# Performance work log

Measured on AMD Instinct MI355X. Metric: run time of the kernel, lower is better.

The kernel has to match this reference:

```python
import jax, jax.numpy as jnp
import numpy as np

N_FFT = 2048
HOP = 512
N_FREQ = N_FFT // 2 + 1  # 1025


def _dft_conv_weights():
    # periodic ('fftbins=True') Hann window, matching librosa get_window('hann', N, fftbins=True)
    n = np.arange(N_FFT)
    win = 0.5 - 0.5 * np.cos(2.0 * np.pi * n / N_FFT)
    k = np.arange(N_FREQ)
    ang = 2.0 * np.pi * np.outer(k, n) / N_FFT  # (F, n_fft)
    # W[n, k] = exp(-2*pi*i*n*k/N); real part = cos, imag part = -sin; windowed per-tap
    w_real = (np.cos(ang) * win[None, :]).astype(np.float32)
    w_imag = (-np.sin(ang) * win[None, :]).astype(np.float32)
    return w_real, w_imag


def setup_inputs() -> dict:
    key = jax.random.key(0)
    x = jax.random.normal(key, (16, 320000), dtype=jnp.float32)
    w_real, w_imag = _dft_conv_weights()
    return {
        "input": x,
        "conv_real_w": jnp.asarray(w_real),
        "conv_imag_w": jnp.asarray(w_imag),
    }


def reference(input, conv_real_w, conv_imag_w):
    # center=True: reflect-pad n_fft//2 on both sides
    pad = N_FFT // 2
    x = jnp.pad(input, ((0, 0), (pad, pad)), mode="reflect")  # (B, L + n_fft)
    L = x.shape[1]
    T = (L - N_FFT) // HOP + 1  # time_steps
    # frame extraction == Conv1d with kernel n_fft, stride hop
    idx = jnp.arange(T)[:, None] * HOP + jnp.arange(N_FFT)[None, :]  # (T, n_fft)
    frames = x[:, idx]  # (B, T, n_fft)
    real = jnp.einsum("btn,fn->bft", frames, conv_real_w)  # (B, F, T)
    imag = jnp.einsum("btn,fn->bft", frames, conv_imag_w)  # (B, F, T)
    return real, imag
```

## Files before the change

kernel.cpp:

```cpp
#include <hip/hip_runtime.h>

#define B_BATCH 16
#define XLEN    320000
#define NFFT    2048
#define HOP     512
#define PADW    1024
#define NFREQ   1025
#define T_OUT   626
#define M_ROWS  2050
#define NCOLS   (B_BATCH * T_OUT)
#define MT2     17
#define NT2     40
#define KT2     32

#define XPAD_LEN    322048
#define XPAD_STRIDE 330240
#define APACK_BYTES ((size_t)MT2 * KT2 * 2 * 8192)
#define XPAD_BYTES  ((size_t)(B_BATCH + 1) * XPAD_STRIDE * 2)
#define WS_NEEDED   (APACK_BYTES + XPAD_BYTES)

typedef __bf16 bf16x8 __attribute__((ext_vector_type(8)));
typedef __bf16 bf16x4 __attribute__((ext_vector_type(4)));
typedef float  f32x4  __attribute__((ext_vector_type(4)));

__device__ __forceinline__ void gload_lds16(const void* g, void* l) {
    __builtin_amdgcn_global_load_lds(
        (const __attribute__((address_space(1))) unsigned int*)g,
        (__attribute__((address_space(3))) unsigned int*)l,
        16, 0, 0);
}

__global__ __launch_bounds__(256) void prep_w(
    const float* __restrict__ wre, const float* __restrict__ wim,
    __bf16* __restrict__ apack)
{
    const int gid   = blockIdx.x * 256 + threadIdx.x;
    const int scell = gid & 3;
    const int row   = (gid >> 2) & 127;
    const int ks    = (gid >> 9) & 1;
    const int kt    = (gid >> 10) & 31;
    const int mt    = gid >> 15;

    const int grow = mt * 128 + row;
    const int k    = kt * 64 + ks * 32 + (((scell ^ (row >> 1)) & 3) << 3);

    bf16x8 v = bf16x8{};
    if (grow < M_ROWS) {
        const float* src = (grow < NFREQ)
            ? (wre + (size_t)grow * NFFT + k)
            : (wim + (size_t)(grow - NFREQ) * NFFT + k);
        const float4 a = *reinterpret_cast<const float4*>(src);
        const float4 b = *reinterpret_cast<const float4*>(src + 4);
        v[0] = (__bf16)a.x; v[1] = (__bf16)a.y; v[2] = (__bf16)a.z; v[3] = (__bf16)a.w;
        v[4] = (__bf16)b.x; v[5] = (__bf16)b.y; v[6] = (__bf16)b.z; v[7] = (__bf16)b.w;
    }
    *reinterpret_cast<bf16x8*>(apack + (size_t)gid * 8) = v;
}

__global__ __launch_bounds__(256) void prep_x(
    const float* __restrict__ x, __bf16* __restrict__ xpad)
{
    const int gid = blockIdx.x * 256 + threadIdx.x;
    if (gid >= (B_BATCH + 1) * (XPAD_STRIDE / 8)) return;
    const int b  = gid / (XPAD_STRIDE / 8);
    const int i0 = (gid - b * (XPAD_STRIDE / 8)) * 8;

    bf16x8 v = bf16x8{};
    if (b < B_BATCH) {
        const float* xb = x + (size_t)b * XLEN;
        const int pos0 = i0 - PADW;
        if (pos0 >= 0 && pos0 + 8 <= XLEN) {
            const float4 a = *reinterpret_cast<const float4*>(xb + pos0);
            const float4 c = *reinterpret_cast<const float4*>(xb + pos0 + 4);
            v[0] = (__bf16)a.x; v[1] = (__bf16)a.y; v[2] = (__bf16)a.z; v[3] = (__bf16)a.w;
            v[4] = (__bf16)c.x; v[5] = (__bf16)c.y; v[6] = (__bf16)c.z; v[7] = (__bf16)c.w;
        } else {
            #pragma unroll
            for (int e = 0; e < 8; ++e) {
                const int i = i0 + e;
                if (i >= XPAD_LEN) { v[e] = (__bf16)0.f; continue; }
                int p = i - PADW;
                p = (p < 0) ? -p : p;
                p = (p >= XLEN) ? (2 * XLEN - 2 - p) : p;
                v[e] = (__bf16)xb[p];
            }
        }
    }
    *reinterpret_cast<bf16x8*>(xpad + (size_t)b * XPAD_STRIDE + i0) = v;
}


#define MFMA16 __builtin_amdgcn_mfma_f32_16x16x32_bf16

#define VM3 asm volatile("s_waitcnt vmcnt(3)" ::: "memory");
#define VM0 asm volatile("s_waitcnt vmcnt(0)" ::: "memory");

#define STG(KT_, KS_, SLOT_) do {                                                  \
    gload_lds16(ablk + (((KT_) * 2 + (KS_)) << 13),                                \
                lds + ((SLOT_) << 13) + (wid << 10));                              \
    {                                                                              \
        const int koff = (KT_) * 128 + (KS_) * 64;                                 \
        unsigned char* d_ = lds + 24576 + ((SLOT_) << 14) + (wid << 10);           \
        gload_lds16(gb0 + koff, d_);                                               \
        gload_lds16(gb1 + koff, d_ + 8192);                                        \
    }                                                                              \
} while (0)

#define PH3(SLOT_, STAGE_, VMW_) do {                                              \
    VMW_                                                                           \
    __builtin_amdgcn_s_barrier();                                                  \
    __builtin_amdgcn_sched_barrier(0);                                             \
    const unsigned abase = ((SLOT_) << 13) + offA_base;                            \
    const unsigned bbase = 24576u + ((SLOT_) << 14) + offB_base;                   \
    bf16x8 a0 = *(const bf16x8*)(lds + abase);                                     \
    bf16x8 a1 = *(const bf16x8*)(lds + abase + 1024);                              \
    bf16x8 a2 = *(const bf16x8*)(lds + abase + 2048);                              \
    bf16x8 a3 = *(const bf16x8*)(lds + abase + 3072);                              \
    bf16x8 b0 = *(const bf16x8*)(lds + bbase);                                     \
    bf16x8 b1 = *(const bf16x8*)(lds + bbase + 1024);                              \
    bf16x8 b2 = *(const bf16x8*)(lds + bbase + 2048);                              \
    bf16x8 b3 = *(const bf16x8*)(lds + bbase + 3072);                              \
    STAGE_                                                                         \
    __builtin_amdgcn_s_setprio(1);                                                 \
    acc[0][0] = MFMA16(a0, b0, acc[0][0], 0, 0, 0);                                \
    acc[0][1] = MFMA16(a0, b1, acc[0][1], 0, 0, 0);                                \
    acc[0][2] = MFMA16(a0, b2, acc[0][2], 0, 0, 0);                                \
    acc[0][3] = MFMA16(a0, b3, acc[0][3], 0, 0, 0);                                \
    acc[1][0] = MFMA16(a1, b0, acc[1][0], 0, 0, 0);                                \
    acc[1][1] = MFMA16(a1, b1, acc[1][1], 0, 0, 0);                                \
    acc[1][2] = MFMA16(a1, b2, acc[1][2], 0, 0, 0);                                \
    acc[1][3] = MFMA16(a1, b3, acc[1][3], 0, 0, 0);                                \
    acc[2][0] = MFMA16(a2, b0, acc[2][0], 0, 0, 0);                                \
    acc[2][1] = MFMA16(a2, b1, acc[2][1], 0, 0, 0);                                \
    acc[2][2] = MFMA16(a2, b2, acc[2][2], 0, 0, 0);                                \
    acc[2][3] = MFMA16(a2, b3, acc[2][3], 0, 0, 0);                                \
    acc[3][0] = MFMA16(a3, b0, acc[3][0], 0, 0, 0);                                \
    acc[3][1] = MFMA16(a3, b1, acc[3][1], 0, 0, 0);                                \
    acc[3][2] = MFMA16(a3, b2, acc[3][2], 0, 0, 0);                                \
    acc[3][3] = MFMA16(a3, b3, acc[3][3], 0, 0, 0);                                \
    __builtin_amdgcn_s_setprio(0);                                                 \
} while (0)

__global__ __launch_bounds__(512, 4) void stft_gemm4(
    const __bf16* __restrict__ apack,
    const __bf16* __restrict__ xpad,
    float* __restrict__ out)
{
    __shared__ __align__(16) unsigned char lds[73728];

    const int tid  = threadIdx.x;
    const int lane = tid & 63;
    const int wid  = tid >> 6;
    const int wm   = wid >> 2;
    const int wn   = wid & 3;
    const int fr   = lane & 15;
    const int kq   = lane >> 4;

    const int orig = (blockIdx.x & 7) * 85 + (blockIdx.x >> 3);
    const int nt = orig / MT2;
    const int mt = orig % MT2;

    const char* ablk = (const char*)apack + (size_t)mt * (KT2 * 2 * 8192) + (size_t)tid * 16;

    const char* xpb = (const char*)xpad;
    const char* gb0;
    const char* gb1;
    {
        const int row0 = tid >> 2;
        const int sc   = ((tid & 3) ^ (row0 >> 1)) & 3;
        int col = nt * 256 + row0;
        unsigned b = (unsigned)col / 626u;
        int tc = col - (int)b * 626;
        gb0 = xpb + ((size_t)b * XPAD_STRIDE + (size_t)tc * 512) * 2 + sc * 16;
        col = nt * 256 + 128 + row0;
        b = (unsigned)col / 626u;
        tc = col - (int)b * 626;
        gb1 = xpb + ((size_t)b * XPAD_STRIDE + (size_t)tc * 512) * 2 + sc * 16;
    }

    const unsigned swz = (unsigned)(((kq ^ (fr >> 1)) & 3) << 4);
    const unsigned offA_base = (unsigned)((wm * 64 + fr) * 64) + swz;
    const unsigned offB_base = (unsigned)((wn * 64 + fr) * 64) + swz;

    f32x4 acc[4][4];
    #pragma unroll
    for (int m = 0; m < 4; ++m)
        #pragma unroll
        for (int n = 0; n < 4; ++n)
            acc[m][n] = f32x4{0.f, 0.f, 0.f, 0.f};

    STG(0, 0, 0);
    STG(0, 1, 1);

    #pragma unroll 1
    for (int i = 0; i < 10; ++i) {
        const int kb = 3 * i;
        PH3(0, STG(kb + 1, 0, 2);, VM3);
        PH3(1, STG(kb + 1, 1, 0);, VM3);
        PH3(2, STG(kb + 2, 0, 1);, VM3);
        PH3(0, STG(kb + 2, 1, 2);, VM3);
        PH3(1, STG(kb + 3, 0, 0);, VM3);
        PH3(2, STG(kb + 3, 1, 1);, VM3);
    }
    PH3(0, STG(31, 0, 2);, VM3);
    PH3(1, STG(31, 1, 0);, VM3);
    PH3(2, , VM3);
    PH3(0, , VM0);

    const size_t imag_base = (size_t)B_BATCH * NFREQ * T_OUT;
    #pragma unroll
    for (int n = 0; n < 4; ++n) {
        const int col = nt * 256 + wn * 64 + n * 16 + fr;
        if (col < NCOLS) {
            const unsigned b = (unsigned)col / 626u;
            const int tc = col - (int)b * 626;
            const size_t colbase = (size_t)b * NFREQ * T_OUT + (size_t)tc;
            #pragma unroll
            for (int m = 0; m < 4; ++m) {
                #pragma unroll
                for (int j = 0; j < 4; ++j) {
                    const int grow = mt * 128 + wm * 64 + m * 16 + kq * 4 + j;
                    if (grow < M_ROWS) {
                        const size_t off = (grow < NFREQ)
                            ? colbase + (size_t)grow * T_OUT
                            : imag_base + colbase + (size_t)(grow - NFREQ) * T_OUT;
                        out[off] = acc[m][n][j];
                    }
                }
            }
        }
    }
}

__device__ __forceinline__ unsigned lds_off_fb(int row, int kbyte) {
    return (unsigned)(row * 128 + (kbyte ^ ((row & 7) << 4)));
}

__global__ __launch_bounds__(256) void stft_gemm_fb(
    const float* __restrict__ x,
    const float* __restrict__ wre,
    const float* __restrict__ wim,
    float* __restrict__ out)
{
    __shared__ __align__(16) unsigned char ldsA[128 * 128];
    __shared__ __align__(16) unsigned char ldsB[128 * 128];

    const int tid  = threadIdx.x;
    const int lane = tid & 63;
    const int wid  = tid >> 6;
    const int wmf  = wid >> 1;
    const int wnf  = wid & 1;

    const int bid = blockIdx.x;
    const int b   = bid / (17 * 5);
    const int rem = bid % (17 * 5);
    const int mt  = rem / 5;
    const int nt  = rem % 5;

    const int row0 = mt * 128;
    const int col0 = nt * 128;
    const float* xb = x + (size_t)b * XLEN;

    const int c4 = (tid & 15) * 4;
    const int r0 = tid >> 4;

    f32x4 acc[4][4];
    #pragma unroll
    for (int m = 0; m < 4; ++m)
        #pragma unroll
        for (int n = 0; n < 4; ++n)
            acc[m][n] = f32x4{0.f, 0.f, 0.f, 0.f};

    const int fr = lane & 15;
    const int kq = lane >> 4;

    for (int k0 = 0; k0 < NFFT; k0 += 64) {
        bf16x4 sa[8], sb[8];
        #pragma unroll
        for (int rr = 0; rr < 8; ++rr) {
            const int row  = rr * 16 + r0;
            const int grow = row0 + row;
            float4 v = make_float4(0.f, 0.f, 0.f, 0.f);
            if (grow < M_ROWS) {
                const float* wsrc = (grow < NFREQ)
                    ? (wre + (size_t)grow * NFFT)
                    : (wim + (size_t)(grow - NFREQ) * NFFT);
                v = *reinterpret_cast<const float4*>(wsrc + k0 + c4);
            }
            sa[rr].x = (__bf16)v.x; sa[rr].y = (__bf16)v.y;
            sa[rr].z = (__bf16)v.z; sa[rr].w = (__bf16)v.w;
        }
        #pragma unroll
        for (int rr = 0; rr < 8; ++rr) {
            const int trow = rr * 16 + r0;
            const int t    = col0 + trow;
            float4 v = make_float4(0.f, 0.f, 0.f, 0.f);
            if (t < T_OUT) {
                const int pos = t * HOP + k0 + c4 - PADW;
                if (pos >= 0 && pos <= XLEN - 4) {
                    v = *reinterpret_cast<const float4*>(xb + pos);
                } else {
                    float tmp[4];
                    #pragma unroll
                    for (int e = 0; e < 4; ++e) {
                        int p = pos + e;
                        p = (p < 0) ? -p : p;
                        p = (p >= XLEN) ? (2 * XLEN - 2 - p) : p;
                        tmp[e] = xb[p];
                    }
                    v = make_float4(tmp[0], tmp[1], tmp[2], tmp[3]);
                }
            }
            sb[rr].x = (__bf16)v.x; sb[rr].y = (__bf16)v.y;
            sb[rr].z = (__bf16)v.z; sb[rr].w = (__bf16)v.w;
        }
        __syncthreads();
        #pragma unroll
        for (int rr = 0; rr < 8; ++rr) {
            const int row = rr * 16 + r0;
            *reinterpret_cast<bf16x4*>(ldsA + lds_off_fb(row, c4 * 2)) = sa[rr];
            *reinterpret_cast<bf16x4*>(ldsB + lds_off_fb(row, c4 * 2)) = sb[rr];
        }
        __syncthreads();
        #pragma unroll
        for (int kk = 0; kk < 2; ++kk) {
            const int kbyte = kk * 64 + kq * 16;
            bf16x8 af[4], bfv[4];
            #pragma unroll
            for (int m = 0; m < 4; ++m)
                af[m] = *reinterpret_cast<const bf16x8*>(
                    ldsA + lds_off_fb(wmf * 64 + m * 16 + fr, kbyte));
            #pragma unroll
            for (int n = 0; n < 4; ++n)
                bfv[n] = *reinterpret_cast<const bf16x8*>(
                    ldsB + lds_off_fb(wnf * 64 + n * 16 + fr, kbyte));
            #pragma unroll
            for (int m = 0; m < 4; ++m)
                #pragma unroll
                for (int n = 0; n < 4; ++n)
                    acc[m][n] = MFMA16(af[m], bfv[n], acc[m][n], 0, 0, 0);
        }
    }

    const size_t imag_base = (size_t)B_BATCH * NFREQ * T_OUT;
    #pragma unroll
    for (int m = 0; m < 4; ++m) {
        #pragma unroll
        for (int n = 0; n < 4; ++n) {
            #pragma unroll
            for (int j = 0; j < 4; ++j) {
                const int grow = row0 + wmf * 64 + m * 16 + kq * 4 + j;
                const int gcol = col0 + wnf * 64 + n * 16 + fr;
                if (grow < M_ROWS && gcol < T_OUT) {
                    size_t off;
                    if (grow < NFREQ)
                        off = ((size_t)b * NFREQ + grow) * T_OUT + gcol;
                    else
                        off = imag_base + ((size_t)b * NFREQ + (grow - NFREQ)) * T_OUT + gcol;
                    out[off] = acc[m][n][j];
                }
            }
        }
    }
}

extern "C" void kernel_launch(void* const* d_in, const int* in_sizes, int n_in,
                              void* d_out, int out_size, void* d_ws, size_t ws_size,
                              hipStream_t stream) {
    const float* x   = (const float*)d_in[0];
    const float* wre = (const float*)d_in[1];
    const float* wim = (const float*)d_in[2];
    float* out = (float*)d_out;

    if (ws_size < WS_NEEDED) {
        stft_gemm_fb<<<dim3(B_BATCH * 17 * 5), 256, 0, stream>>>(x, wre, wim, out);
        return;
    }

    __bf16* apack = (__bf16*)d_ws;
    __bf16* xpad  = (__bf16*)((char*)d_ws + APACK_BYTES);

    prep_w<<<dim3(557056 / 256), 256, 0, stream>>>(wre, wim, apack);
    prep_x<<<dim3(((B_BATCH + 1) * (XPAD_STRIDE / 8) + 255) / 256), 256, 0, stream>>>(x, xpad);
    stft_gemm4<<<dim3(MT2 * NT2), 512, 0, stream>>>(apack, xpad, out);
}
```

Measured before the change: 112.9 us.

## Shrink GEMM tile to 128x128 with register double-buffered LDS fragments

Replaces the 512-thread 128x256 tile kernel with a 256-thread 128x128 tile kernel that grids 17x79 blocks. Each block has a 3-slot LDS ring of 32-wide K phases, and fragments are prefetched into alternating register sets so LDS reads of the next phase overlap the current MFMA cluster. The weight packing layout changes to match, and the block-to-XCD mapping is remapped for the new grid size. The aim is better load balance across CUs and more overlap between LDS reads and MFMA. The cost is more blocks, twice the A-tile reloads from global memory, and higher register pressure from the double fragment sets.

```diff
diff --git a/kernel.cpp b/kernel.cpp
--- a/kernel.cpp
+++ b/kernel.cpp
@@ -10,7 +10,8 @@
 #define M_ROWS  2050
 #define NCOLS   (B_BATCH * T_OUT)
 #define MT2     17
-#define NT2     40
+#define NT3     79
+#define NBLK    (MT2 * NT3)
 #define KT2     32
 
 #define XPAD_LEN    322048
@@ -37,12 +38,11 @@
     const int gid   = blockIdx.x * 256 + threadIdx.x;
     const int scell = gid & 3;
     const int row   = (gid >> 2) & 127;
-    const int ks    = (gid >> 9) & 1;
-    const int kt    = (gid >> 10) & 31;
+    const int ph    = (gid >> 9) & 63;
     const int mt    = gid >> 15;
 
     const int grow = mt * 128 + row;
-    const int k    = kt * 64 + ks * 32 + (((scell ^ (row >> 1)) & 3) << 3);
+    const int k    = ph * 32 + (((scell ^ (row >> 1)) & 3) << 3);
 
     bf16x8 v = bf16x8{};
     if (grow < M_ROWS) {
@@ -92,87 +92,102 @@
 
 #define MFMA16 __builtin_amdgcn_mfma_f32_16x16x32_bf16
 
-#define VM3 asm volatile("s_waitcnt vmcnt(3)" ::: "memory");
+#define VM4 asm volatile("s_waitcnt vmcnt(4)" ::: "memory");
 #define VM0 asm volatile("s_waitcnt vmcnt(0)" ::: "memory");
 
-#define STG(KT_, KS_, SLOT_) do {                                                  \
-    gload_lds16(ablk + (((KT_) * 2 + (KS_)) << 13),                                \
-                lds + ((SLOT_) << 13) + (wid << 10));                              \
-    {                                                                              \
-        const int koff = (KT_) * 128 + (KS_) * 64;                                 \
-        unsigned char* d_ = lds + 24576 + ((SLOT_) << 14) + (wid << 10);           \
-        gload_lds16(gb0 + koff, d_);                                               \
-        gload_lds16(gb1 + koff, d_ + 8192);                                        \
-    }                                                                              \
-} while (0)
-
-#define PH3(SLOT_, STAGE_, VMW_) do {                                              \
-    VMW_                                                                           \
-    __builtin_amdgcn_s_barrier();                                                  \
-    __builtin_amdgcn_sched_barrier(0);                                             \
-    const unsigned abase = ((SLOT_) << 13) + offA_base;                            \
-    const unsigned bbase = 24576u + ((SLOT_) << 14) + offB_base;                   \
-    bf16x8 a0 = *(const bf16x8*)(lds + abase);                                     \
-    bf16x8 a1 = *(const bf16x8*)(lds + abase + 1024);                              \
-    bf16x8 a2 = *(const bf16x8*)(lds + abase + 2048);                              \
-    bf16x8 a3 = *(const bf16x8*)(lds + abase + 3072);                              \
-    bf16x8 b0 = *(const bf16x8*)(lds + bbase);                                     \
-    bf16x8 b1 = *(const bf16x8*)(lds + bbase + 1024);                              \
-    bf16x8 b2 = *(const bf16x8*)(lds + bbase + 2048);                              \
-    bf16x8 b3 = *(const bf16x8*)(lds + bbase + 3072);                              \
-    STAGE_                                                                         \
-    __builtin_amdgcn_s_setprio(1);                                                 \
-    acc[0][0] = MFMA16(a0, b0, acc[0][0], 0, 0, 0);                                \
-    acc[0][1] = MFMA16(a0, b1, acc[0][1], 0, 0, 0);                                \
-    acc[0][2] = MFMA16(a0, b2, acc[0][2], 0, 0, 0);                                \
-    acc[0][3] = MFMA16(a0, b3, acc[0][3], 0, 0, 0);                                \
-    acc[1][0] = MFMA16(a1, b0, acc[1][0], 0, 0, 0);                                \
-    acc[1][1] = MFMA16(a1, b1, acc[1][1], 0, 0, 0);                                \
-    acc[1][2] = MFMA16(a1, b2, acc[1][2], 0, 0, 0);                                \
-    acc[1][3] = MFMA16(a1, b3, acc[1][3], 0, 0, 0);                                \
-    acc[2][0] = MFMA16(a2, b0, acc[2][0], 0, 0, 0);                                \
-    acc[2][1] = MFMA16(a2, b1, acc[2][1], 0, 0, 0);                                \
-    acc[2][2] = MFMA16(a2, b2, acc[2][2], 0, 0, 0);                                \
-    acc[2][3] = MFMA16(a2, b3, acc[2][3], 0, 0, 0);                                \
-    acc[3][0] = MFMA16(a3, b0, acc[3][0], 0, 0, 0);                                \
-    acc[3][1] = MFMA16(a3, b1, acc[3][1], 0, 0, 0);                                \
-    acc[3][2] = MFMA16(a3, b2, acc[3][2], 0, 0, 0);                                \
-    acc[3][3] = MFMA16(a3, b3, acc[3][3], 0, 0, 0);                                \
-    __builtin_amdgcn_s_setprio(0);                                                 \
-} while (0)
-
-__global__ __launch_bounds__(512, 4) void stft_gemm4(
+#define STGM(PH_, SLOT_) {                                                        \
+    const char* as_ = ablk + ((size_t)(PH_) << 13);                               \
+    unsigned char* ad_ = lds + ((SLOT_) << 13) + (wid << 11);                     \
+    gload_lds16(as_, ad_);                                                        \
+    gload_lds16(as_ + 1024, ad_ + 1024);                                          \
+    const int ko_ = (PH_) << 6;                                                   \
+    unsigned char* bd_ = lds + 24576 + ((SLOT_) << 13) + (wid << 11);             \
+    gload_lds16(gb0 + ko_, bd_);                                                  \
+    gload_lds16(gb1 + ko_, bd_ + 1024);                                           \
+}
+
+#define MFMA_CLUSTER(A0,A1,A2,A3,B0,B1,B2,B3)                                     \
+    acc[0][0] = MFMA16(A0, B0, acc[0][0], 0, 0, 0);                               \
+    acc[0][1] = MFMA16(A0, B1, acc[0][1], 0, 0, 0);                               \
+    acc[0][2] = MFMA16(A0, B2, acc[0][2], 0, 0, 0);                               \
+    acc[0][3] = MFMA16(A0, B3, acc[0][3], 0, 0, 0);                               \
+    acc[1][0] = MFMA16(A1, B0, acc[1][0], 0, 0, 0);                               \
+    acc[1][1] = MFMA16(A1, B1, acc[1][1], 0, 0, 0);                               \
+    acc[1][2] = MFMA16(A1, B2, acc[1][2], 0, 0, 0);                               \
+    acc[1][3] = MFMA16(A1, B3, acc[1][3], 0, 0, 0);                               \
+    acc[2][0] = MFMA16(A2, B0, acc[2][0], 0, 0, 0);                               \
+    acc[2][1] = MFMA16(A2, B1, acc[2][1], 0, 0, 0);                               \
+    acc[2][2] = MFMA16(A2, B2, acc[2][2], 0, 0, 0);                               \
+    acc[2][3] = MFMA16(A2, B3, acc[2][3], 0, 0, 0);                               \
+    acc[3][0] = MFMA16(A3, B0, acc[3][0], 0, 0, 0);                               \
+    acc[3][1] = MFMA16(A3, B1, acc[3][1], 0, 0, 0);                               \
+    acc[3][2] = MFMA16(A3, B2, acc[3][2], 0, 0, 0);                               \
+    acc[3][3] = MFMA16(A3, B3, acc[3][3], 0, 0, 0);
+
+#define PHASE(SLN_, STG_, VMW_, CA0,CA1,CA2,CA3,CB0,CB1,CB2,CB3,                  \
+              NA0,NA1,NA2,NA3,NB0,NB1,NB2,NB3) {                                  \
+    STG_                                                                          \
+    VMW_                                                                          \
+    __builtin_amdgcn_s_barrier();                                                 \
+    __builtin_amdgcn_sched_barrier(0);                                            \
+    {                                                                             \
+        const unsigned ab_ = ((unsigned)(SLN_) << 13) + offA_base;                \
+        const unsigned bb_ = ((unsigned)(SLN_) << 13) + offB_base;                \
+        NA0 = *(const bf16x8*)(lds + ab_);                                        \
+        NA1 = *(const bf16x8*)(lds + ab_ + 1024);                                 \
+        NA2 = *(const bf16x8*)(lds + ab_ + 2048);                                 \
+        NA3 = *(const bf16x8*)(lds + ab_ + 3072);                                 \
+        NB0 = *(const bf16x8*)(lds + bb_);                                        \
+        NB1 = *(const bf16x8*)(lds + bb_ + 1024);                                 \
+        NB2 = *(const bf16x8*)(lds + bb_ + 2048);                                 \
+        NB3 = *(const bf16x8*)(lds + bb_ + 3072);                                 \
+    }                                                                             \
+    __builtin_amdgcn_s_setprio(1);                                                \
+    MFMA_CLUSTER(CA0,CA1,CA2,CA3,CB0,CB1,CB2,CB3)                                 \
+    __builtin_amdgcn_s_setprio(0);                                                \
+    asm volatile("s_waitcnt lgkmcnt(0)" ::: "memory");                            \
+    __builtin_amdgcn_sched_barrier(0);                                            \
+}
+
+__global__ __launch_bounds__(256, 3) void stft_gemm5(
     const __bf16* __restrict__ apack,
     const __bf16* __restrict__ xpad,
     float* __restrict__ out)
 {
-    __shared__ __align__(16) unsigned char lds[73728];
+    __shared__ __align__(16) unsigned char lds[49152];
 
     const int tid  = threadIdx.x;
     const int lane = tid & 63;
     const int wid  = tid >> 6;
-    const int wm   = wid >> 2;
-    const int wn   = wid & 3;
+    const int wm   = wid >> 1;
+    const int wn   = wid & 1;
     const int fr   = lane & 15;
     const int kq   = lane >> 4;
 
-    const int orig = (blockIdx.x & 7) * 85 + (blockIdx.x >> 3);
-    const int nt = orig / MT2;
-    const int mt = orig % MT2;
-
-    const char* ablk = (const char*)apack + (size_t)mt * (KT2 * 2 * 8192) + (size_t)tid * 16;
+    int G;
+    {
+        const int L = blockIdx.x;
+        const int xcd = L & 7;
+        const int pos = L >> 3;
+        G = (xcd < 7) ? xcd * 168 + pos : 1176 + pos;
+    }
+    const int mt = G / NT3;
+    const int nt = G - mt * NT3;
+
+    const char* ablk = (const char*)apack + (size_t)mt * (64 * 8192)
+                       + (wid << 11) + (lane << 4);
 
     const char* xpb = (const char*)xpad;
     const char* gb0;
     const char* gb1;
     {
-        const int row0 = tid >> 2;
-        const int sc   = ((tid & 3) ^ (row0 >> 1)) & 3;
-        int col = nt * 256 + row0;
+        const int r0 = wid * 32 + (lane >> 2);
+        const int sc = (lane & 3) ^ ((r0 >> 1) & 3);
+        int col = nt * 128 + r0;
         unsigned b = (unsigned)col / 626u;
         int tc = col - (int)b * 626;
         gb0 = xpb + ((size_t)b * XPAD_STRIDE + (size_t)tc * 512) * 2 + sc * 16;
-        col = nt * 256 + 128 + row0;
+        col += 16;
         b = (unsigned)col / 626u;
         tc = col - (int)b * 626;
         gb1 = xpb + ((size_t)b * XPAD_STRIDE + (size_t)tc * 512) * 2 + sc * 16;
@@ -180,7 +195,7 @@
 
     const unsigned swz = (unsigned)(((kq ^ (fr >> 1)) & 3) << 4);
     const unsigned offA_base = (unsigned)((wm * 64 + fr) * 64) + swz;
-    const unsigned offB_base = (unsigned)((wn * 64 + fr) * 64) + swz;
+    const unsigned offB_base = 24576u + (unsigned)((wn * 64 + fr) * 64) + swz;
 
     f32x4 acc[4][4];
     #pragma unroll
@@ -189,28 +204,59 @@
         for (int n = 0; n < 4; ++n)
             acc[m][n] = f32x4{0.f, 0.f, 0.f, 0.f};
 
-    STG(0, 0, 0);
-    STG(0, 1, 1);
+    bf16x8 pa0, pa1, pa2, pa3, pb0, pb1, pb2, pb3;
+    bf16x8 qa0, qa1, qa2, qa3, qb0, qb1, qb2, qb3;
+
+    STGM(0, 0)
+    STGM(1, 1)
+    VM4
+    __builtin_amdgcn_s_barrier();
+    __builtin_amdgcn_sched_barrier(0);
+    {
+        const unsigned ab_ = offA_base;
+        const unsigned bb_ = offB_base;
+        pa0 = *(const bf16x8*)(lds + ab_);
+        pa1 = *(const bf16x8*)(lds + ab_ + 1024);
+        pa2 = *(const bf16x8*)(lds + ab_ + 2048);
+        pa3 = *(const bf16x8*)(lds + ab_ + 3072);
+        pb0 = *(const bf16x8*)(lds + bb_);
+        pb1 = *(const bf16x8*)(lds + bb_ + 1024);
+        pb2 = *(const bf16x8*)(lds + bb_ + 2048);
+        pb3 = *(const bf16x8*)(lds + bb_ + 3072);
+    }
+    asm volatile("s_waitcnt lgkmcnt(0)" ::: "memory");
+    __builtin_amdgcn_sched_barrier(0);
 
     #pragma unroll 1
     for (int i = 0; i < 10; ++i) {
-        const int kb = 3 * i;
-        PH3(0, STG(kb + 1, 0, 2);, VM3);
-        PH3(1, STG(kb + 1, 1, 0);, VM3);
-        PH3(2, STG(kb + 2, 0, 1);, VM3);
-        PH3(0, STG(kb + 2, 1, 2);, VM3);
-        PH3(1, STG(kb + 3, 0, 0);, VM3);
-        PH3(2, STG(kb + 3, 1, 1);, VM3);
-    }
-    PH3(0, STG(31, 0, 2);, VM3);
-    PH3(1, STG(31, 1, 0);, VM3);
-    PH3(2, , VM3);
-    PH3(0, , VM0);
+        const int t = 6 * i;
+        PHASE(1, STGM(t + 2, 2), VM4, pa0,pa1,pa2,pa3,pb0,pb1,pb2,pb3,
+                                       qa0,qa1,qa2,qa3,qb0,qb1,qb2,qb3)
+        PHASE(2, STGM(t + 3, 0), VM4, qa0,qa1,qa2,qa3,qb0,qb1,qb2,qb3,
+                                       pa0,pa1,pa2,pa3,pb0,pb1,pb2,pb3)
+        PHASE(0, STGM(t + 4, 1), VM4, pa0,pa1,pa2,pa3,pb0,pb1,pb2,pb3,
+                                       qa0,qa1,qa2,qa3,qb0,qb1,qb2,qb3)
+        PHASE(1, STGM(t + 5, 2), VM4, qa0,qa1,qa2,qa3,qb0,qb1,qb2,qb3,
+                                       pa0,pa1,pa2,pa3,pb0,pb1,pb2,pb3)
+        PHASE(2, STGM(t + 6, 0), VM4, pa0,pa1,pa2,pa3,pb0,pb1,pb2,pb3,
+                                       qa0,qa1,qa2,qa3,qb0,qb1,qb2,qb3)
+        PHASE(0, STGM(t + 7, 1), VM4, qa0,qa1,qa2,qa3,qb0,qb1,qb2,qb3,
+                                       pa0,pa1,pa2,pa3,pb0,pb1,pb2,pb3)
+    }
+    PHASE(1, STGM(62, 2), VM4, pa0,pa1,pa2,pa3,pb0,pb1,pb2,pb3,
+                                qa0,qa1,qa2,qa3,qb0,qb1,qb2,qb3)
+    PHASE(2, STGM(63, 0), VM4, qa0,qa1,qa2,qa3,qb0,qb1,qb2,qb3,
+                                pa0,pa1,pa2,pa3,pb0,pb1,pb2,pb3)
+    PHASE(0, , VM0,            pa0,pa1,pa2,pa3,pb0,pb1,pb2,pb3,
+                                qa0,qa1,qa2,qa3,qb0,qb1,qb2,qb3)
+    __builtin_amdgcn_s_setprio(1);
+    MFMA_CLUSTER(qa0,qa1,qa2,qa3,qb0,qb1,qb2,qb3)
+    __builtin_amdgcn_s_setprio(0);
 
     const size_t imag_base = (size_t)B_BATCH * NFREQ * T_OUT;
     #pragma unroll
     for (int n = 0; n < 4; ++n) {
-        const int col = nt * 256 + wn * 64 + n * 16 + fr;
+        const int col = nt * 128 + wn * 64 + n * 16 + fr;
         if (col < NCOLS) {
             const unsigned b = (unsigned)col / 626u;
             const int tc = col - (int)b * 626;
@@ -382,5 +428,5 @@
 
     prep_w<<<dim3(557056 / 256), 256, 0, stream>>>(wre, wim, apack);
     prep_x<<<dim3(((B_BATCH + 1) * (XPAD_STRIDE / 8) + 255) / 256), 256, 0, stream>>>(x, xpad);
-    stft_gemm4<<<dim3(MT2 * NT2), 512, 0, stream>>>(apack, xpad, out);
-}
+    stft_gemm5<<<dim3(NBLK), 256, 0, stream>>>(apack, xpad, out);
+}
```

Result: slower. 152.6 us (+35.1%).
